# Kernel tuning notes

Measured on AMD Instinct MI355X. Metric: run time of the kernel, lower is better.

Reference implementation:

```python
import jax, jax.numpy as jnp
import numpy as np

# physical / init constants (from DPINeuron.__init__ with default 1e-12 currents)
I0 = 5e-13
UT = 0.025
KAPPA = (0.75 + 0.66) / 2  # 0.705
CMEM, CAMPA, CSHUNT = 3e-12, 2e-12, 2e-12
ITAU_MEM = 1e-12
IGAIN_MEM = 1e-12
ITAU_AMPA = 1e-12
IGAIN_AMPA = 1e-12
ITH = 1e-12
IPFB_TH = 1e-12
IPFB_NORM = 1e-12
REFP = 0.0
DT = 0.001
TAU_MEM = UT / KAPPA * CMEM / ITAU_MEM
TAU_AMPA = UT / KAPPA * CAMPA / ITAU_AMPA
TAU_SHUNT = UT / KAPPA * CSHUNT / ITAU_AMPA
SLOPE = 25.0  # fast_sigmoid surrogate slope

@jax.custom_vjp
def ste_round(x):
    return jnp.round(x)

def _round_fwd(x):
    return jnp.round(x), None

def _round_bwd(_, g):
    return (g,)  # straight-through estimator

ste_round.defvjp(_round_fwd, _round_bwd)

@jax.custom_vjp
def fast_sigmoid(x):
    return (x > 0).astype(x.dtype)

def _fs_fwd(x):
    return (x > 0).astype(x.dtype), x

def _fs_bwd(x, g):
    return (g / (SLOPE * jnp.abs(x) + 1.0) ** 2,)

fast_sigmoid.defvjp(_fs_fwd, _fs_bwd)

B, N_IN, N_OUT = 4096, 2048, 2048

def setup_inputs() -> dict:
    key = jax.random.key(0)
    k1, = jax.random.split(key, 1)
    X = (jax.random.uniform(k1, (B, N_IN), dtype=jnp.float32) < 0.1).astype(jnp.float32)  # sparse input spikes
    return {
        "X": X,
        "W_ampa": jnp.ones((N_OUT, N_IN), jnp.float32),   # init.constant_(1.0)
        "W_shunt": jnp.ones((N_OUT, N_IN), jnp.float32),
        "Imem": jnp.full((B, N_OUT), I0, jnp.float32),    # initialize(): zeros + I0
        "Iampa": jnp.full((B, N_OUT), I0, jnp.float32),
        "Ishunt": jnp.full((B, N_OUT), I0, jnp.float32),
        "refractory": jnp.zeros((B, N_OUT), jnp.float32),
        "Idc": jnp.float32(1e-12),
        "Iw_ampa": jnp.float32(1e-12),
        "Iw_shunt": jnp.float32(1e-12),
        "alpha": jnp.float32(IGAIN_MEM / ITAU_MEM),       # 1.0
        "beta": jnp.float32(1.0 + I0 / ITAU_MEM),         # 1.5
    }

def reference(X, W_ampa, W_shunt, Imem, Iampa, Ishunt, refractory,
              Idc, Iw_ampa, Iw_shunt, alpha, beta):
    Iahp = I0
    Inmda = I0
    # synapse projections with STE-rounded weights: [B, n_out]
    numSynAmpa = jnp.einsum('bi,oi->bo', X, ste_round(W_ampa))
    numSynShunt = jnp.einsum('bi,oi->bo', X, ste_round(W_shunt))

    dIampa = -Iampa / TAU_AMPA
    Iampa = Iampa + (IGAIN_AMPA / ITAU_AMPA) * Iw_ampa * numSynAmpa
    dIshunt = -Ishunt / TAU_SHUNT
    Ishunt = Ishunt + (IGAIN_AMPA / ITAU_AMPA) * Iw_shunt * numSynShunt

    Iin = Idc + Iampa + Inmda - Ishunt
    Iin = Iin * (refractory <= 0)
    Iin = jnp.maximum(Iin, I0)

    Ifb = (I0 ** (1.0 / (KAPPA + 1.0))) * Imem ** (KAPPA / (KAPPA + 1.0)) \
          / (1.0 + jnp.exp(-IPFB_NORM * (Imem - IPFB_TH)))
    f_imem = Ifb / ITAU_MEM * (Imem + IGAIN_MEM)
    dImem = (alpha * (Iin - ITAU_MEM - Iahp) - beta * Imem
             + jax.lax.stop_gradient(f_imem)) / (TAU_MEM * (1.0 + IGAIN_MEM / Imem))
    Imem = jnp.maximum(Imem + dImem * DT, I0)

    # note: original code applies dIshunt decay to Iampa (kept faithful)
    Iampa = jnp.maximum(Iampa + dIampa * DT, I0)
    Iampa = jnp.maximum(Iampa + dIshunt * DT, I0)

    spike = fast_sigmoid(Imem - ITH)
    Imem = (1.0 - spike) * Imem + spike * I0
    refractory = jnp.maximum(refractory - DT, 0.0)
    refractory = (1.0 - spike) * refractory + spike * REFP
    return spike, Imem, Iampa, Ishunt, refractory
```

## Files before the change

### kernel.cpp

```cpp
#include <hip/hip_runtime.h>
#include <cmath>

#ifndef __has_builtin
#define __has_builtin(x) 0
#endif

#define B_DIM 4096
#define K_DIM 2048
#define N_DIM 2048

#define BM 128
#define BN 128
#define BK 64

typedef __attribute__((ext_vector_type(4))) float f32x4;
typedef __attribute__((ext_vector_type(4))) int i32x4;
typedef __attribute__((ext_vector_type(16))) signed char i8x16;


__device__ __forceinline__ signed char f2i8(float f) {
    int t = __float2int_rn(f);
    t = t < -127 ? -127 : (t > 127 ? 127 : t);
    return (signed char)t;
}

__device__ __forceinline__ void gl2lds16(const void* g, void* l) {
#if __has_builtin(__builtin_amdgcn_global_load_lds)
    __builtin_amdgcn_global_load_lds((__attribute__((address_space(1))) void*)g,
                                     (__attribute__((address_space(3))) void*)l,
                                     16, 0, 0);
#else
    *(uint4*)l = *(const uint4*)g;
#endif
}

#define VMWAIT0   asm volatile("s_waitcnt vmcnt(0)" ::: "memory")
#define FENCE     asm volatile("" ::: "memory")
#define SBARRIER  do { FENCE; __builtin_amdgcn_s_barrier(); FENCE; } while (0)


__global__ void cast_x_kernel(const float* __restrict__ X,
                              signed char* __restrict__ Xb) {
    size_t i = ((size_t)blockIdx.x * 256 + threadIdx.x) * 16;
    i8x16 o;
#pragma unroll
    for (int j = 0; j < 16; j += 4) {
        f32x4 a = *(const f32x4*)(X + i + j);
        o[j]     = f2i8(a[0]);
        o[j + 1] = f2i8(a[1]);
        o[j + 2] = f2i8(a[2]);
        o[j + 3] = f2i8(a[3]);
    }
    *(i8x16*)(Xb + i) = o;
}

__global__ void cast_w_kernel(const float* __restrict__ Wa,
                              const float* __restrict__ Ws,
                              signed char* __restrict__ Wab,
                              signed char* __restrict__ Wsb) {
    size_t i = ((size_t)blockIdx.x * 256 + threadIdx.x) * 16;
    i8x16 oa, os;
#pragma unroll
    for (int j = 0; j < 16; j += 4) {
        f32x4 a = *(const f32x4*)(Wa + i + j);
        f32x4 s = *(const f32x4*)(Ws + i + j);
        oa[j]     = f2i8(a[0]); oa[j + 1] = f2i8(a[1]);
        oa[j + 2] = f2i8(a[2]); oa[j + 3] = f2i8(a[3]);
        os[j]     = f2i8(s[0]); os[j + 1] = f2i8(s[1]);
        os[j + 2] = f2i8(s[2]); os[j + 3] = f2i8(s[3]);
    }
    *(i8x16*)(Wab + i) = oa;
    *(i8x16*)(Wsb + i) = os;
}


#define RS 132

__device__ __forceinline__ void stage_tile(int tt, int tid, int m0, int n0,
                                           unsigned char* smem,
                                           const signed char* __restrict__ Xb,
                                           const signed char* __restrict__ Wab,
                                           const signed char* __restrict__ Wsb) {
    unsigned char* bb = smem + (tt & 1) * 24576;
    const int k0s = tt * BK;
#pragma unroll
    for (int j = 0; j < 2; j++) {
        const int c   = j * 256 + tid;
        const int row = c >> 2;
        const int js  = (c & 3) ^ ((row >> 1) & 3);
        gl2lds16(Xb + (size_t)(m0 + row) * K_DIM + k0s + js * 16, bb + c * 16);
    }
#pragma unroll
    for (int j = 0; j < 2; j++) {
        const int c   = j * 256 + tid;
        const int row = c >> 2;
        const int js  = (c & 3) ^ ((row >> 1) & 3);
        const size_t go = (size_t)(n0 + row) * K_DIM + k0s + js * 16;
        gl2lds16(Wab + go, bb + 8192  + c * 16);
        gl2lds16(Wsb + go, bb + 16384 + c * 16);
    }
}

__global__ __launch_bounds__(256, 2)
void dpi_fused_kernel(const signed char* __restrict__ Xb,
                      const signed char* __restrict__ Wab,
                      const signed char* __restrict__ Wsb,
                      const float* __restrict__ gImem,
                      const float* __restrict__ gIampa,
                      const float* __restrict__ gIshunt,
                      const float* __restrict__ gRefr,
                      const float* __restrict__ pIdc,
                      const float* __restrict__ pIwa,
                      const float* __restrict__ pIws,
                      const float* __restrict__ pAlpha,
                      const float* __restrict__ pBeta,
                      float* __restrict__ out,
                      float i0pow, float kexp, float tau_mem, float inv_tau_syn)
{
    __shared__ __align__(16) unsigned char smem[49152];
    float* na_buf = (float*)smem;
    float* ns_buf = (float*)(smem + 16896);

    const int tid  = threadIdx.x;
    const int lane = tid & 63;
    const int wave = tid >> 6;

    const int lin = blockIdx.x;
    const int xcd = lin & 7;
    const int loc = lin >> 3;
    const int mb  = (xcd & 3) * 8 + (loc & 7);
    const int nb  = (xcd >> 2) * 8 + (loc >> 3);
    const int m0  = mb * BM;
    const int n0  = nb * BN;

    const int wm = (wave & 1) * 64;
    const int wn = (wave >> 1) * 64;

    i32x4 accA[4][4], accS[4][4];
#pragma unroll
    for (int i = 0; i < 4; i++)
#pragma unroll
        for (int j = 0; j < 4; j++) { accA[i][j] = (i32x4)0; accS[i][j] = (i32x4)0; }

    const int frow   = lane & 15;
    const int kq     = lane >> 4;
    const int slot16 = (kq ^ ((frow >> 1) & 3)) * 16;

    stage_tile(0, tid, m0, n0, smem, Xb, Wab, Wsb);
    VMWAIT0; SBARRIER;

#pragma unroll 2
    for (int t = 0; t < 32; ++t) {
        const unsigned char* bb = smem + (t & 1) * 24576;
        const signed char* sA  = (const signed char*)bb;
        const signed char* sWa = (const signed char*)(bb + 8192);
        const signed char* sWs = (const signed char*)(bb + 16384);

        i32x4 af[4], ba[4], bs[4];
#pragma unroll
        for (int mi = 0; mi < 4; mi++)
            af[mi] = *(const i32x4*)(sA + (wm + mi * 16 + frow) * 64 + slot16);
#pragma unroll
        for (int ni = 0; ni < 4; ni++) {
            const int o = (wn + ni * 16 + frow) * 64 + slot16;
            ba[ni] = *(const i32x4*)(sWa + o);
            bs[ni] = *(const i32x4*)(sWs + o);
        }

        if (t < 31) stage_tile(t + 1, tid, m0, n0, smem, Xb, Wab, Wsb);
        __builtin_amdgcn_sched_barrier(0);

#pragma unroll
        for (int mi = 0; mi < 4; mi++)
#pragma unroll
            for (int ni = 0; ni < 4; ni++) {
                accA[mi][ni] = __builtin_amdgcn_mfma_i32_16x16x64_i8(af[mi], ba[ni], accA[mi][ni], 0, 0, 0);
                accS[mi][ni] = __builtin_amdgcn_mfma_i32_16x16x64_i8(af[mi], bs[ni], accS[mi][ni], 0, 0, 0);
            }

        VMWAIT0; SBARRIER;
    }

    const float idc   = *pIdc;
    const float iwa   = *pIwa;
    const float iws   = *pIws;
    const float alpha = *pAlpha;
    const float beta  = *pBeta;

    const size_t plane = (size_t)B_DIM * N_DIM;
    float* __restrict__ oSpike = out;
    float* __restrict__ oImem  = out + plane;
    float* __restrict__ oIampa = out + 2 * plane;
    float* __restrict__ oIsh   = out + 3 * plane;
    float* __restrict__ oRefr  = out + 4 * plane;

    const int rowgroup = wm >> 6;
    const int quad4    = (lane >> 4) << 2;
    const int cseg     = (tid & 31) * 4;
    const int rgrp     = tid >> 5;

#pragma unroll
    for (int s = 0; s < 4; s++) {
#pragma unroll
        for (int ni = 0; ni < 4; ni++) {
            const int lcol = wn + ni * 16 + (lane & 15);
#pragma unroll
            for (int r = 0; r < 4; r++) {
                const int lrow = rowgroup * 16 + quad4 + r;
                na_buf[lrow * RS + lcol] = (float)accA[s][ni][r];
                ns_buf[lrow * RS + lcol] = (float)accS[s][ni][r];
            }
        }
        __syncthreads();

#pragma unroll
        for (int q = 0; q < 4; q++) {
            const int lrow = rgrp * 4 + q;
            const int grow = m0 + (lrow >> 4) * 64 + s * 16 + (lrow & 15);
            const size_t idx = (size_t)grow * N_DIM + n0 + cseg;

            const f32x4 na4 = *(const f32x4*)(na_buf + lrow * RS + cseg);
            const f32x4 ns4 = *(const f32x4*)(ns_buf + lrow * RS + cseg);
            const f32x4 im4 = *(const f32x4*)(gImem   + idx);
            const f32x4 ia4 = *(const f32x4*)(gIampa  + idx);
            const f32x4 is4 = *(const f32x4*)(gIshunt + idx);
            const f32x4 rf4 = *(const f32x4*)(gRefr   + idx);

            f32x4 sp_o, im_o, ia_o, is_o, rf_o;
#pragma unroll
            for (int e = 0; e < 4; e++) {
                const float na  = na4[e];
                const float ns  = ns4[e];
                const float im  = im4[e];
                const float ia  = ia4[e];
                const float ish = is4[e];
                const float rf  = rf4[e];

                const float dIampa  = -ia * inv_tau_syn;
                const float ia2     = ia + iwa * na;
                const float dIshunt = -ish * inv_tau_syn;
                const float ish2    = ish + iws * ns;

                float Iin = idc + ia2 + 5e-13f - ish2;
                Iin = (rf <= 0.0f) ? Iin : 0.0f;
                Iin = fmaxf(Iin, 5e-13f);

                const float ifb = i0pow *
                    __builtin_amdgcn_exp2f(kexp * __builtin_amdgcn_logf(im)) * 0.5f;
                const float fimem = ifb * 1e12f * (im + 1e-12f);
                const float dImem = (alpha * ((Iin - 1e-12f) - 5e-13f) - beta * im + fimem)
                                    / (tau_mem * (1.0f + 1e-12f / im));
                float im2 = fmaxf(im + dImem * 0.001f, 5e-13f);

                float ia3 = fmaxf(ia2 + dIampa * 0.001f, 5e-13f);
                ia3       = fmaxf(ia3 + dIshunt * 0.001f, 5e-13f);

                const float spike = (im2 - 1e-12f > 0.0f) ? 1.0f : 0.0f;
                im2 = (spike > 0.0f) ? 5e-13f : im2;
                float rf2 = fmaxf(rf - 0.001f, 0.0f);
                rf2 = (spike > 0.0f) ? 0.0f : rf2;

                sp_o[e] = spike; im_o[e] = im2; ia_o[e] = ia3;
                is_o[e] = ish2;  rf_o[e] = rf2;
            }

            *(f32x4*)(oSpike + idx) = sp_o;
            *(f32x4*)(oImem  + idx) = im_o;
            *(f32x4*)(oIampa + idx) = ia_o;
            *(f32x4*)(oIsh   + idx) = is_o;
            *(f32x4*)(oRefr  + idx) = rf_o;
        }
        __syncthreads();
    }
}


extern "C" void kernel_launch(void* const* d_in, const int* in_sizes, int n_in,
                              void* d_out, int out_size, void* d_ws, size_t ws_size,
                              hipStream_t stream) {
    (void)in_sizes; (void)n_in; (void)out_size; (void)ws_size;

    const float* X       = (const float*)d_in[0];
    const float* W_ampa  = (const float*)d_in[1];
    const float* W_shunt = (const float*)d_in[2];
    const float* Imem    = (const float*)d_in[3];
    const float* Iampa   = (const float*)d_in[4];
    const float* Ishunt  = (const float*)d_in[5];
    const float* Refr    = (const float*)d_in[6];
    const float* pIdc    = (const float*)d_in[7];
    const float* pIwa    = (const float*)d_in[8];
    const float* pIws    = (const float*)d_in[9];
    const float* pAlpha  = (const float*)d_in[10];
    const float* pBeta   = (const float*)d_in[11];

    signed char* Xb  = (signed char*)d_ws;
    signed char* Wab = Xb  + (size_t)B_DIM * K_DIM;
    signed char* Wsb = Wab + (size_t)N_DIM * K_DIM;

    const float i0pow       = (float)std::pow(5e-13, 1.0 / 1.705);
    const float kexp        = (float)(0.705 / 1.705);
    const float tau_mem     = (float)(0.025 / 0.705 * 3.0);
    const float inv_tau_syn = (float)(1.0 / (0.025 / 0.705 * 2.0));

    cast_x_kernel<<<dim3((B_DIM * K_DIM) / (256 * 16)), dim3(256), 0, stream>>>(X, Xb);
    cast_w_kernel<<<dim3((N_DIM * K_DIM) / (256 * 16)), dim3(256), 0, stream>>>(
        W_ampa, W_shunt, Wab, Wsb);

    dpi_fused_kernel<<<dim3(512), dim3(256), 0, stream>>>(
        Xb, Wab, Wsb, Imem, Iampa, Ishunt, Refr,
        pIdc, pIwa, pIws, pAlpha, pBeta,
        (float*)d_out, i0pow, kexp, tau_mem, inv_tau_syn);
}
```

Before: 357.6 us.

## Triple-buffer LDS tiles with prefetch distance two and partial vmcnt waits

Replaces the double-buffered K loop with a three-buffer LDS ring that prefetches two tiles ahead. It waits with vmcnt(6) so only the oldest tile's global-to-LDS loads must land before each step. The aim is to hide global load latency behind more MFMA work instead of draining all loads each iteration. In exchange, LDS per block grows from 48KB to 72KB, which may limit occupancy at two blocks per CU, and the loop is manually unrolled in groups of three.

```diff
diff --git a/kernel.cpp b/kernel.cpp
--- a/kernel.cpp
+++ b/kernel.cpp
@@ -34,9 +34,10 @@
 #endif
 }
 
-#define VMWAIT0   asm volatile("s_waitcnt vmcnt(0)" ::: "memory")
-#define FENCE     asm volatile("" ::: "memory")
-#define SBARRIER  do { FENCE; __builtin_amdgcn_s_barrier(); FENCE; } while (0)
+#define VMWAIT_(n) asm volatile("s_waitcnt vmcnt(" #n ")" ::: "memory")
+#define VMWAIT(n)  VMWAIT_(n)
+#define FENCE      asm volatile("" ::: "memory")
+#define SBARRIER   do { FENCE; __builtin_amdgcn_s_barrier(); FENCE; } while (0)
 
 
 __global__ void cast_x_kernel(const float* __restrict__ X,
@@ -76,12 +77,12 @@
 
 #define RS 132
 
-__device__ __forceinline__ void stage_tile(int tt, int tid, int m0, int n0,
+__device__ __forceinline__ void stage_tile(int tt, int bufIdx, int tid, int m0, int n0,
                                            unsigned char* smem,
                                            const signed char* __restrict__ Xb,
                                            const signed char* __restrict__ Wab,
                                            const signed char* __restrict__ Wsb) {
-    unsigned char* bb = smem + (tt & 1) * 24576;
+    unsigned char* bb = smem + bufIdx * 24576;
     const int k0s = tt * BK;
 #pragma unroll
     for (int j = 0; j < 2; j++) {
@@ -99,6 +100,30 @@
         gl2lds16(Wab + go, bb + 8192  + c * 16);
         gl2lds16(Wsb + go, bb + 16384 + c * 16);
     }
+}
+
+#define TILE_STEP(t_, rb_, sb_, WAITN, DOSTG)                                 \
+{                                                                             \
+  VMWAIT(WAITN); SBARRIER;                                                    \
+  const unsigned char* bb = smem + (rb_) * 24576;                             \
+  const signed char* sA  = (const signed char*)bb;                            \
+  const signed char* sWa = (const signed char*)(bb + 8192);                   \
+  const signed char* sWs = (const signed char*)(bb + 16384);                  \
+  i32x4 af[4], ba[4], bs[4];                                                  \
+  _Pragma("unroll") for (int mi = 0; mi < 4; mi++)                            \
+      af[mi] = *(const i32x4*)(sA + (wm + mi * 16 + frow) * 64 + slot16);     \
+  _Pragma("unroll") for (int ni = 0; ni < 4; ni++) {                          \
+      const int o = (wn + ni * 16 + frow) * 64 + slot16;                      \
+      ba[ni] = *(const i32x4*)(sWa + o);                                      \
+      bs[ni] = *(const i32x4*)(sWs + o);                                      \
+  }                                                                           \
+  if (DOSTG) stage_tile((t_) + 2, (sb_), tid, m0, n0, smem, Xb, Wab, Wsb);    \
+  __builtin_amdgcn_sched_barrier(0);                                          \
+  _Pragma("unroll") for (int mi = 0; mi < 4; mi++)                            \
+  _Pragma("unroll") for (int ni = 0; ni < 4; ni++) {                          \
+      accA[mi][ni] = __builtin_amdgcn_mfma_i32_16x16x64_i8(af[mi], ba[ni], accA[mi][ni], 0, 0, 0); \
+      accS[mi][ni] = __builtin_amdgcn_mfma_i32_16x16x64_i8(af[mi], bs[ni], accS[mi][ni], 0, 0, 0); \
+  }                                                                           \
 }
 
 __global__ __launch_bounds__(256, 2)
@@ -117,7 +142,7 @@
                       float* __restrict__ out,
                       float i0pow, float kexp, float tau_mem, float inv_tau_syn)
 {
-    __shared__ __align__(16) unsigned char smem[49152];
+    __shared__ __align__(16) unsigned char smem[73728];
     float* na_buf = (float*)smem;
     float* ns_buf = (float*)(smem + 16896);
 
@@ -146,40 +171,18 @@
     const int kq     = lane >> 4;
     const int slot16 = (kq ^ ((frow >> 1) & 3)) * 16;
 
-    stage_tile(0, tid, m0, n0, smem, Xb, Wab, Wsb);
-    VMWAIT0; SBARRIER;
-
-#pragma unroll 2
-    for (int t = 0; t < 32; ++t) {
-        const unsigned char* bb = smem + (t & 1) * 24576;
-        const signed char* sA  = (const signed char*)bb;
-        const signed char* sWa = (const signed char*)(bb + 8192);
-        const signed char* sWs = (const signed char*)(bb + 16384);
-
-        i32x4 af[4], ba[4], bs[4];
-#pragma unroll
-        for (int mi = 0; mi < 4; mi++)
-            af[mi] = *(const i32x4*)(sA + (wm + mi * 16 + frow) * 64 + slot16);
-#pragma unroll
-        for (int ni = 0; ni < 4; ni++) {
-            const int o = (wn + ni * 16 + frow) * 64 + slot16;
-            ba[ni] = *(const i32x4*)(sWa + o);
-            bs[ni] = *(const i32x4*)(sWs + o);
-        }
-
-        if (t < 31) stage_tile(t + 1, tid, m0, n0, smem, Xb, Wab, Wsb);
-        __builtin_amdgcn_sched_barrier(0);
-
-#pragma unroll
-        for (int mi = 0; mi < 4; mi++)
-#pragma unroll
-            for (int ni = 0; ni < 4; ni++) {
-                accA[mi][ni] = __builtin_amdgcn_mfma_i32_16x16x64_i8(af[mi], ba[ni], accA[mi][ni], 0, 0, 0);
-                accS[mi][ni] = __builtin_amdgcn_mfma_i32_16x16x64_i8(af[mi], bs[ni], accS[mi][ni], 0, 0, 0);
-            }
-
-        VMWAIT0; SBARRIER;
-    }
+    stage_tile(0, 0, tid, m0, n0, smem, Xb, Wab, Wsb); FENCE;
+    stage_tile(1, 1, tid, m0, n0, smem, Xb, Wab, Wsb); FENCE;
+
+    for (int tb = 0; tb < 30; tb += 3) {
+        TILE_STEP(tb + 0, 0, 2, 6, 1);
+        TILE_STEP(tb + 1, 1, 0, 6, 1);
+        TILE_STEP(tb + 2, 2, 1, 6, 1);
+    }
+    TILE_STEP(30, 0, 2, 6, 0);
+    TILE_STEP(31, 1, 0, 0, 0);
+
+    SBARRIER;
 
     const float idc   = *pIdc;
     const float iwa   = *pIwa;
```

Result: no change. 364.7 us (+2.0%).
